# Performance work log

Hardware: AMD Instinct MI355X
Metric: run time of the kernel (lower is better)

The kernel has to match this reference:

```python
import jax, jax.numpy as jnp
import numpy as np

BN_EPS = 1e-5

def setup_inputs() -> dict:
    key = jax.random.key(0)
    k1, k2 = jax.random.split(key)
    B, C, H, W, K = 256, 2048, 7, 7, 16
    featmap = jax.random.normal(k1, (B, C, H, W), dtype=jnp.float32)
    w16 = jax.random.normal(k2, (K, C), dtype=jnp.float32) * 0.02  # 1x1 conv weight
    bn_gamma = jnp.ones((K,), jnp.float32)
    bn_beta = jnp.zeros((K,), jnp.float32)
    bn_mean = jnp.zeros((K,), jnp.float32)
    bn_var = jnp.ones((K,), jnp.float32)
    return {"featmap": featmap, "w16": w16, "bn_gamma": bn_gamma,
            "bn_beta": bn_beta, "bn_mean": bn_mean, "bn_var": bn_var}

def reference(featmap, w16, bn_gamma, bn_beta, bn_mean, bn_var):
    # featmap: [B, 2048, 7, 7]; 1x1 conv -> featcov16: [B, 16, 7, 7]
    featcov16 = jnp.einsum('bchw,kc->bkhw', featmap, w16)
    # BatchNorm2d(16), inference-style with running stats
    inv = bn_gamma / jnp.sqrt(bn_var + BN_EPS)
    featcov16 = featcov16 * inv[None, :, None, None] + (bn_beta - bn_mean * inv)[None, :, None, None]
    # Loop-free bilinear pooling: original repeats featcov16[:,i] to 2048 ch,
    # multiplies with featmap, and AvgPool2d(7) -> mean over HxW.
    HW = featmap.shape[2] * featmap.shape[3]
    feat_matrix = jnp.einsum('bkhw,bchw->bkc', featcov16, featmap) / HW  # [B,16,2048]
    bp_out_feat = feat_matrix.reshape(feat_matrix.shape[0], -1)  # [B, 32768]
    return bp_out_feat
```

## Files before the change

kernel.cpp:

```cpp
#include <hip/hip_runtime.h>

#define BATCH 256
#define CDIM  2048
#define HW    49
#define KDIM  16
#define CHUNK 512
#define TILE  128
#define ROWP  52

__global__ __launch_bounds__(256) void pconv_kernel(
    const float* __restrict__ fm, const float* __restrict__ w16,
    float* __restrict__ Ppart)
{
    __shared__ __align__(16) float fm_t[TILE * ROWP + 16];
    __shared__ __align__(16) float w_t[TILE * KDIM];

    const int tid = threadIdx.x;
    const int b   = blockIdx.x >> 2;
    const int q   = blockIdx.x & 3;
    const int c0  = q * CHUNK;
    const int h4  = tid & 15;
    const int cs  = tid >> 4;

    float acc[KDIM][4];
    #pragma unroll
    for (int k = 0; k < KDIM; ++k) {
        acc[k][0] = 0.f; acc[k][1] = 0.f; acc[k][2] = 0.f; acc[k][3] = 0.f;
    }

    const float* fmb = fm + (size_t)b * CDIM * HW;

    for (int tile = 0; tile < CHUNK / TILE; ++tile) {
        const int ct = c0 + tile * TILE;
        __syncthreads();
        const float4* src = (const float4*)(fmb + ct * HW);
        for (int i = tid; i < (TILE * HW) / 4; i += 256) {
            float4 v = src[i];
            int e = i * 4;
            int cl = e / HW; int h = e - cl * HW; fm_t[cl * ROWP + h] = v.x;
            e++; cl = e / HW; h = e - cl * HW;    fm_t[cl * ROWP + h] = v.y;
            e++; cl = e / HW; h = e - cl * HW;    fm_t[cl * ROWP + h] = v.z;
            e++; cl = e / HW; h = e - cl * HW;    fm_t[cl * ROWP + h] = v.w;
        }
        for (int i = tid; i < KDIM * TILE; i += 256) {
            int kk = i >> 7; int cc = i & 127;
            w_t[cc * KDIM + kk] = w16[kk * CDIM + ct + cc];
        }
        __syncthreads();
        #pragma unroll 2
        for (int j = 0; j < 8; ++j) {
            const int cc = cs * 8 + j;
            float4 f = *(const float4*)&fm_t[cc * ROWP + 4 * h4];
            const float4* wq = (const float4*)&w_t[cc * KDIM];
            float wv[16];
            *(float4*)&wv[0]  = wq[0];
            *(float4*)&wv[4]  = wq[1];
            *(float4*)&wv[8]  = wq[2];
            *(float4*)&wv[12] = wq[3];
            #pragma unroll
            for (int k = 0; k < 16; ++k) {
                acc[k][0] += wv[k] * f.x;
                acc[k][1] += wv[k] * f.y;
                acc[k][2] += wv[k] * f.z;
                acc[k][3] += wv[k] * f.w;
            }
        }
    }

    __syncthreads();
    float* red = fm_t;
    for (int r = 0; r < 4; ++r) {
        #pragma unroll
        for (int kk = 0; kk < 4; ++kk)
            #pragma unroll
            for (int hl = 0; hl < 4; ++hl)
                red[cs * 272 + h4 * 17 + kk * 4 + hl] = acc[r * 4 + kk][hl];
        __syncthreads();
        const int kp = r * 4 + (tid >> 6);
        const int hw = tid & 63;
        if (hw < HW) {
            float s = 0.f;
            const int base = (hw >> 2) * 17 + (tid >> 6) * 4 + (hw & 3);
            #pragma unroll
            for (int c = 0; c < 16; ++c) s += red[c * 272 + base];
            Ppart[(size_t)blockIdx.x * 784 + kp * HW + hw] = s;
        }
        __syncthreads();
    }
}

__global__ __launch_bounds__(256) void bp_kernel(
    const float* __restrict__ fm, const float* __restrict__ Ppart,
    const float* __restrict__ gamma, const float* __restrict__ beta,
    const float* __restrict__ mean, const float* __restrict__ var,
    float* __restrict__ out)
{
    __shared__ __align__(16) float Pt[HW * KDIM];
    __shared__ __align__(16) float fm_s[256 * HW];

    const int tid = threadIdx.x;
    const int b   = blockIdx.x >> 3;
    const int c0  = (blockIdx.x & 7) * 256;

    for (int p = tid; p < 784; p += 256) {
        const float* pp = Ppart + (size_t)(b * 4) * 784 + p;
        float s = pp[0] + pp[784] + pp[1568] + pp[2352];
        int kk = p / HW; int hw = p - kk * HW;
        float inv   = gamma[kk] * rsqrtf(var[kk] + 1e-5f);
        float shift = beta[kk] - mean[kk] * inv;
        Pt[hw * KDIM + kk] = (s * inv + shift) * (1.0f / 49.0f);
    }

    {
        const float4* src = (const float4*)(fm + ((size_t)b * CDIM + c0) * HW);
        float4* dst = (float4*)fm_s;
        #pragma unroll 7
        for (int i = tid; i < (256 * HW) / 4; i += 256) dst[i] = src[i];
    }
    __syncthreads();

    float acc[16];
    #pragma unroll
    for (int i = 0; i < 16; ++i) acc[i] = 0.f;

    const float* row = fm_s + tid * HW;
    #pragma unroll 7
    for (int hw = 0; hw < HW; ++hw) {
        float f = row[hw];
        const float4* pv = (const float4*)&Pt[hw * KDIM];
        float4 p0 = pv[0], p1 = pv[1], p2 = pv[2], p3 = pv[3];
        acc[0]  += p0.x * f; acc[1]  += p0.y * f; acc[2]  += p0.z * f; acc[3]  += p0.w * f;
        acc[4]  += p1.x * f; acc[5]  += p1.y * f; acc[6]  += p1.z * f; acc[7]  += p1.w * f;
        acc[8]  += p2.x * f; acc[9]  += p2.y * f; acc[10] += p2.z * f; acc[11] += p2.w * f;
        acc[12] += p3.x * f; acc[13] += p3.y * f; acc[14] += p3.z * f; acc[15] += p3.w * f;
    }

    float* ob = out + (size_t)b * (KDIM * CDIM) + c0 + tid;
    #pragma unroll
    for (int kk = 0; kk < 16; ++kk) ob[kk * CDIM] = acc[kk];
}

extern "C" void kernel_launch(void* const* d_in, const int* in_sizes, int n_in,
                              void* d_out, int out_size, void* d_ws, size_t ws_size,
                              hipStream_t stream) {
    const float* fm    = (const float*)d_in[0];
    const float* w16   = (const float*)d_in[1];
    const float* gamma = (const float*)d_in[2];
    const float* beta  = (const float*)d_in[3];
    const float* mean  = (const float*)d_in[4];
    const float* var   = (const float*)d_in[5];
    float* out   = (float*)d_out;
    float* Ppart = (float*)d_ws;

    pconv_kernel<<<BATCH * 4, 256, 0, stream>>>(fm, w16, Ppart);
    bp_kernel<<<BATCH * 8, 256, 0, stream>>>(fm, Ppart, gamma, beta, mean, var, out);
}
```

Measured before the change: 213.2 us.

## Fuse conv and bilinear pooling into one per-batch kernel with register prefetch

```diff
diff --git a/kernel.cpp b/kernel.cpp
--- a/kernel.cpp
+++ b/kernel.cpp
@@ -4,23 +4,31 @@
 #define CDIM  2048
 #define HW    49
 #define KDIM  16
-#define CHUNK 512
-#define TILE  128
-#define ROWP  52
 
-__global__ __launch_bounds__(256) void pconv_kernel(
+#define NT     512
+#define TILE   128
+#define NTILE  (CDIM/TILE)
+#define RED_H  37
+#define RED_CS (16*RED_H)
+#define CHUNK2 512
+
+__global__ __launch_bounds__(NT) void fused_kernel(
     const float* __restrict__ fm, const float* __restrict__ w16,
-    float* __restrict__ Ppart)
+    const float* __restrict__ gamma, const float* __restrict__ beta,
+    const float* __restrict__ mean, const float* __restrict__ var,
+    float* __restrict__ out)
 {
-    __shared__ __align__(16) float fm_t[TILE * ROWP + 16];
-    __shared__ __align__(16) float w_t[TILE * KDIM];
+    __shared__ __align__(16) float big[CHUNK2 * HW];
+    __shared__ __align__(16) float fmt[TILE * HW + 32];
+    __shared__ __align__(16) float wt[TILE * KDIM];
+    __shared__ __align__(16) float Pt[HW * KDIM];
 
     const int tid = threadIdx.x;
-    const int b   = blockIdx.x >> 2;
-    const int q   = blockIdx.x & 3;
-    const int c0  = q * CHUNK;
-    const int h4  = tid & 15;
-    const int cs  = tid >> 4;
+    const int b   = blockIdx.x;
+    const float* __restrict__ fmb = fm + (size_t)b * CDIM * HW;
+
+    const int h4 = tid & 15;
+    const int cs = tid >> 4;
 
     float acc[KDIM][4];
     #pragma unroll
@@ -28,116 +36,121 @@
         acc[k][0] = 0.f; acc[k][1] = 0.f; acc[k][2] = 0.f; acc[k][3] = 0.f;
     }
 
-    const float* fmb = fm + (size_t)b * CDIM * HW;
+    for (int i = tid; i < TILE * KDIM; i += NT) {
+        const int kk = i & 15, cl = i >> 4;
+        wt[i] = w16[kk * CDIM + cl];
+    }
+    {
+        const float4* src = (const float4*)fmb;
+        float4* dst = (float4*)fmt;
+        for (int i = tid; i < (TILE * HW) / 4; i += NT) dst[i] = src[i];
+    }
 
-    for (int tile = 0; tile < CHUNK / TILE; ++tile) {
-        const int ct = c0 + tile * TILE;
+    const bool has4 = (tid < (TILE * HW) / 4 - 3 * NT);
+
+    for (int t = 0; t < NTILE; ++t) {
         __syncthreads();
-        const float4* src = (const float4*)(fmb + ct * HW);
-        for (int i = tid; i < (TILE * HW) / 4; i += 256) {
-            float4 v = src[i];
-            int e = i * 4;
-            int cl = e / HW; int h = e - cl * HW; fm_t[cl * ROWP + h] = v.x;
-            e++; cl = e / HW; h = e - cl * HW;    fm_t[cl * ROWP + h] = v.y;
-            e++; cl = e / HW; h = e - cl * HW;    fm_t[cl * ROWP + h] = v.z;
-            e++; cl = e / HW; h = e - cl * HW;    fm_t[cl * ROWP + h] = v.w;
+
+        float4 pf0, pf1, pf2, pf3;
+        float  wp0, wp1, wp2, wp3;
+        if (t < NTILE - 1) {
+            const float4* nsrc = (const float4*)(fmb + (t + 1) * TILE * HW);
+            pf0 = nsrc[tid]; pf1 = nsrc[tid + NT]; pf2 = nsrc[tid + 2 * NT];
+            if (has4) pf3 = nsrc[tid + 3 * NT];
+            const int nct = (t + 1) * TILE;
+            {
+                int i = tid;          wp0 = w16[(i & 15) * CDIM + nct + (i >> 4)];
+                i = tid + NT;         wp1 = w16[(i & 15) * CDIM + nct + (i >> 4)];
+                i = tid + 2 * NT;     wp2 = w16[(i & 15) * CDIM + nct + (i >> 4)];
+                i = tid + 3 * NT;     wp3 = w16[(i & 15) * CDIM + nct + (i >> 4)];
+            }
         }
-        for (int i = tid; i < KDIM * TILE; i += 256) {
-            int kk = i >> 7; int cc = i & 127;
-            w_t[cc * KDIM + kk] = w16[kk * CDIM + ct + cc];
-        }
-        __syncthreads();
-        #pragma unroll 2
-        for (int j = 0; j < 8; ++j) {
-            const int cc = cs * 8 + j;
-            float4 f = *(const float4*)&fm_t[cc * ROWP + 4 * h4];
-            const float4* wq = (const float4*)&w_t[cc * KDIM];
+
+        #pragma unroll
+        for (int j = 0; j < TILE / 32; ++j) {
+            const int cc = cs + 32 * j;
+            const float* fr = fmt + cc * HW + 4 * h4;
+            const float f0 = fr[0], f1 = fr[1], f2 = fr[2], f3 = fr[3];
+            const float4* wq = (const float4*)(wt + cc * KDIM);
             float wv[16];
             *(float4*)&wv[0]  = wq[0];
             *(float4*)&wv[4]  = wq[1];
             *(float4*)&wv[8]  = wq[2];
             *(float4*)&wv[12] = wq[3];
             #pragma unroll
-            for (int k = 0; k < 16; ++k) {
-                acc[k][0] += wv[k] * f.x;
-                acc[k][1] += wv[k] * f.y;
-                acc[k][2] += wv[k] * f.z;
-                acc[k][3] += wv[k] * f.w;
+            for (int k = 0; k < KDIM; ++k) {
+                acc[k][0] += wv[k] * f0;
+                acc[k][1] += wv[k] * f1;
+                acc[k][2] += wv[k] * f2;
+                acc[k][3] += wv[k] * f3;
+            }
+        }
+
+        __syncthreads();
+        if (t < NTILE - 1) {
+            float4* dst = (float4*)fmt;
+            dst[tid] = pf0; dst[tid + NT] = pf1; dst[tid + 2 * NT] = pf2;
+            if (has4) dst[tid + 3 * NT] = pf3;
+            wt[tid] = wp0; wt[tid + NT] = wp1; wt[tid + 2 * NT] = wp2; wt[tid + 3 * NT] = wp3;
+        }
+    }
+
+    {
+        float* red = big;
+        const int kw  = tid >> 6;
+        const int hw2 = tid & 63;
+        const int rb  = (hw2 >> 2) * RED_H + kw * 4 + (hw2 & 3);
+        #pragma unroll
+        for (int r = 0; r < 2; ++r) {
+            __syncthreads();
+            #pragma unroll
+            for (int kk = 0; kk < 8; ++kk) {
+                #pragma unroll
+                for (int e = 0; e < 4; ++e)
+                    red[cs * RED_CS + h4 * RED_H + kk * 4 + e] = acc[r * 8 + kk][e];
+            }
+            __syncthreads();
+            if (hw2 < HW) {
+                float s = 0.f;
+                #pragma unroll
+                for (int c = 0; c < 32; ++c) s += red[c * RED_CS + rb];
+                const int k = r * 8 + kw;
+                const float inv   = gamma[k] * rsqrtf(var[k] + 1e-5f);
+                const float shift = beta[k] - mean[k] * inv;
+                Pt[hw2 * KDIM + k] = (s * inv + shift) * (1.0f / 49.0f);
             }
         }
     }
 
-    __syncthreads();
-    float* red = fm_t;
-    for (int r = 0; r < 4; ++r) {
-        #pragma unroll
-        for (int kk = 0; kk < 4; ++kk)
-            #pragma unroll
-            for (int hl = 0; hl < 4; ++hl)
-                red[cs * 272 + h4 * 17 + kk * 4 + hl] = acc[r * 4 + kk][hl];
+    for (int ch = 0; ch < CDIM / CHUNK2; ++ch) {
         __syncthreads();
-        const int kp = r * 4 + (tid >> 6);
-        const int hw = tid & 63;
-        if (hw < HW) {
-            float s = 0.f;
-            const int base = (hw >> 2) * 17 + (tid >> 6) * 4 + (hw & 3);
-            #pragma unroll
-            for (int c = 0; c < 16; ++c) s += red[c * 272 + base];
-            Ppart[(size_t)blockIdx.x * 784 + kp * HW + hw] = s;
+        {
+            const float4* src = (const float4*)(fmb + ch * CHUNK2 * HW);
+            float4* dst = (float4*)big;
+            for (int i = tid; i < (CHUNK2 * HW) / 4; i += NT) dst[i] = src[i];
         }
         __syncthreads();
+
+        float a[KDIM];
+        #pragma unroll
+        for (int k = 0; k < KDIM; ++k) a[k] = 0.f;
+
+        const float* row = big + tid * HW;
+        #pragma unroll 7
+        for (int hw = 0; hw < HW; ++hw) {
+            const float f = row[hw];
+            const float4* pv = (const float4*)(Pt + hw * KDIM);
+            const float4 p0 = pv[0], p1 = pv[1], p2 = pv[2], p3 = pv[3];
+            a[0]  += p0.x * f; a[1]  += p0.y * f; a[2]  += p0.z * f; a[3]  += p0.w * f;
+            a[4]  += p1.x * f; a[5]  += p1.y * f; a[6]  += p1.z * f; a[7]  += p1.w * f;
+            a[8]  += p2.x * f; a[9]  += p2.y * f; a[10] += p2.z * f; a[11] += p2.w * f;
+            a[12] += p3.x * f; a[13] += p3.y * f; a[14] += p3.z * f; a[15] += p3.w * f;
+        }
+
+        float* ob = out + (size_t)b * (KDIM * CDIM) + ch * CHUNK2 + tid;
+        #pragma unroll
+        for (int k = 0; k < KDIM; ++k) ob[k * CDIM] = a[k];
     }
-}
-
-__global__ __launch_bounds__(256) void bp_kernel(
-    const float* __restrict__ fm, const float* __restrict__ Ppart,
-    const float* __restrict__ gamma, const float* __restrict__ beta,
-    const float* __restrict__ mean, const float* __restrict__ var,
-    float* __restrict__ out)
-{
-    __shared__ __align__(16) float Pt[HW * KDIM];
-    __shared__ __align__(16) float fm_s[256 * HW];
-
-    const int tid = threadIdx.x;
-    const int b   = blockIdx.x >> 3;
-    const int c0  = (blockIdx.x & 7) * 256;
-
-    for (int p = tid; p < 784; p += 256) {
-        const float* pp = Ppart + (size_t)(b * 4) * 784 + p;
-        float s = pp[0] + pp[784] + pp[1568] + pp[2352];
-        int kk = p / HW; int hw = p - kk * HW;
-        float inv   = gamma[kk] * rsqrtf(var[kk] + 1e-5f);
-        float shift = beta[kk] - mean[kk] * inv;
-        Pt[hw * KDIM + kk] = (s * inv + shift) * (1.0f / 49.0f);
-    }
-
-    {
-        const float4* src = (const float4*)(fm + ((size_t)b * CDIM + c0) * HW);
-        float4* dst = (float4*)fm_s;
-        #pragma unroll 7
-        for (int i = tid; i < (256 * HW) / 4; i += 256) dst[i] = src[i];
-    }
-    __syncthreads();
-
-    float acc[16];
-    #pragma unroll
-    for (int i = 0; i < 16; ++i) acc[i] = 0.f;
-
-    const float* row = fm_s + tid * HW;
-    #pragma unroll 7
-    for (int hw = 0; hw < HW; ++hw) {
-        float f = row[hw];
-        const float4* pv = (const float4*)&Pt[hw * KDIM];
-        float4 p0 = pv[0], p1 = pv[1], p2 = pv[2], p3 = pv[3];
-        acc[0]  += p0.x * f; acc[1]  += p0.y * f; acc[2]  += p0.z * f; acc[3]  += p0.w * f;
-        acc[4]  += p1.x * f; acc[5]  += p1.y * f; acc[6]  += p1.z * f; acc[7]  += p1.w * f;
-        acc[8]  += p2.x * f; acc[9]  += p2.y * f; acc[10] += p2.z * f; acc[11] += p2.w * f;
-        acc[12] += p3.x * f; acc[13] += p3.y * f; acc[14] += p3.z * f; acc[15] += p3.w * f;
-    }
-
-    float* ob = out + (size_t)b * (KDIM * CDIM) + c0 + tid;
-    #pragma unroll
-    for (int kk = 0; kk < 16; ++kk) ob[kk * CDIM] = acc[kk];
 }
 
 extern "C" void kernel_launch(void* const* d_in, const int* in_sizes, int n_in,
@@ -149,9 +162,8 @@
     const float* beta  = (const float*)d_in[3];
     const float* mean  = (const float*)d_in[4];
     const float* var   = (const float*)d_in[5];
-    float* out   = (float*)d_out;
-    float* Ppart = (float*)d_ws;
+    float* out = (float*)d_out;
+    (void)d_ws; (void)ws_size;
 
-    pconv_kernel<<<BATCH * 4, 256, 0, stream>>>(fm, w16, Ppart);
-    bp_kernel<<<BATCH * 8, 256, 0, stream>>>(fm, Ppart, gamma, beta, mean, var, out);
+    fused_kernel<<<BATCH, NT, 0, stream>>>(fm, w16, gamma, beta, mean, var, out);
 }
```

After: 209.3 us. Within noise of the previous version (-1.8%).
